# Optimization experiments

Measured on AMD Instinct MI355X. Metric: run time of the kernel, lower is better.

The kernel has to match this reference:

```python
import jax, jax.numpy as jnp
import numpy as np

N = 65536      # nodes (256x256 grid)
E = 1048576    # edges (avg degree 16)
T_IN = 10      # TIME_STEPS_IN
L = 64         # LATENT_DIMS
MID = 128      # LATENT_DIMS * MLP_RATIO
GD = 2         # grid dims


def _lin_init(key, fan_in, fan_out):
    kw, kb = jax.random.split(key)
    s = 1.0 / np.sqrt(fan_in)
    W = jax.random.uniform(kw, (fan_in, fan_out), jnp.float32, -s, s)
    b = jax.random.uniform(kb, (fan_out,), jnp.float32, -s, s)
    return W, b


def setup_inputs() -> dict:
    key = jax.random.key(0)
    ks = jax.random.split(key, 10)
    x = jax.random.normal(ks[0], (N, T_IN), jnp.float32)
    grid = jax.random.uniform(ks[1], (N, GD), jnp.float32)
    edge_index = jax.random.randint(ks[2], (2, E), 0, N, jnp.int64)
    W_proj1, b_proj1 = _lin_init(ks[3], T_IN + GD, MID)
    W_proj2, b_proj2 = _lin_init(ks[4], MID, L)
    Wk, bk = _lin_init(ks[5], 2 * L + 2 * GD + 1, L)   # K edge MLP (single linear)
    Ww, bw = _lin_init(ks[6], L, L)                     # W node MLP (single linear)
    W_dec1, b_dec1 = _lin_init(ks[7], L, MID)
    W_dec2, b_dec2 = _lin_init(ks[8], MID, 1)
    return {"x": x, "grid": grid, "edge_index": edge_index,
            "W_proj1": W_proj1, "b_proj1": b_proj1, "W_proj2": W_proj2, "b_proj2": b_proj2,
            "Wk": Wk, "bk": bk, "Ww": Ww, "bw": bw,
            "W_dec1": W_dec1, "b_dec1": b_dec1, "W_dec2": W_dec2, "b_dec2": b_dec2}


def _gelu(x):
    return jax.nn.gelu(x, approximate=False)  # torch F.gelu default = exact erf


def reference(x, grid, edge_index, W_proj1, b_proj1, W_proj2, b_proj2,
              Wk, bk, Ww, bw, W_dec1, b_dec1, W_dec2, b_dec2):
    # project: cat(x, grid) -> Linear -> GELU -> Linear
    h = jnp.concatenate([x, grid], axis=-1)               # [N, T_IN+2]
    h = _gelu(h @ W_proj1 + b_proj1) @ W_proj2 + b_proj2  # [N, L]

    # message passing block (PyG source_to_target: j = row 0, i = row 1)
    src = edge_index[0]
    dst = edge_index[1]
    x_j = h[src]                                          # [E, L]
    x_i = h[dst]                                          # [E, L]
    g_j = grid[src]                                       # [E, 2]
    g_i = grid[dst]                                       # [E, 2]
    dist = jnp.sqrt(jnp.sum(jnp.square(g_i - g_j), axis=-1, keepdims=True))  # [E, 1]
    ef = jnp.concatenate([dist, g_i, g_j, x_i, x_j], axis=-1)  # [E, 2L+5]
    msg = ef @ Wk + bk                                    # [E, L]
    aggr = jax.ops.segment_sum(msg, dst, num_segments=N)  # [N, L]
    h = _gelu(h @ Ww + bw + aggr)                         # update

    # decode: Linear -> GELU -> Linear
    out = _gelu(h @ W_dec1 + b_dec1) @ W_dec2 + b_dec2    # [N, 1]
    return out
```

## Files before the change

kernel.cpp:

```cpp
#include <hip/hip_runtime.h>
#include <hip/hip_fp16.h>

static __device__ __forceinline__ float gelu(float x) {
    return 0.5f * x * (1.0f + erff(x * 0.70710678118654752f));
}

#define CAPR 32

typedef _Float16 v8h __attribute__((ext_vector_type(8)));
typedef float    v4f __attribute__((ext_vector_type(4)));
typedef int      v4i __attribute__((ext_vector_type(4)));
union F8 { uint4 u; v8h v; _Float16 f[8]; };

static __device__ __forceinline__ void acc8(float* a, uint4 u) {
    float2 f0 = __half22float2(*(__half2*)&u.x);
    float2 f1 = __half22float2(*(__half2*)&u.y);
    float2 f2 = __half22float2(*(__half2*)&u.z);
    float2 f3 = __half22float2(*(__half2*)&u.w);
    a[0] += f0.x; a[1] += f0.y; a[2] += f1.x; a[3] += f1.y;
    a[4] += f2.x; a[5] += f2.y; a[6] += f3.x; a[7] += f3.y;
}

static __device__ __forceinline__ uint4 pack8(const float* v) {
    __half2 p0 = __floats2half2_rn(v[0], v[1]);
    __half2 p1 = __floats2half2_rn(v[2], v[3]);
    __half2 p2 = __floats2half2_rn(v[4], v[5]);
    __half2 p3 = __floats2half2_rn(v[6], v[7]);
    uint4 u;
    u.x = *(unsigned*)&p0; u.y = *(unsigned*)&p1;
    u.z = *(unsigned*)&p2; u.w = *(unsigned*)&p3;
    return u;
}

__global__ void __launch_bounds__(256, 4)
k_enc_scat(const float* __restrict__ x,
           const float* __restrict__ grid,
           const float* __restrict__ W1,
           const float* __restrict__ b1,
           const float* __restrict__ W2,
           const float* __restrict__ b2,
           const int* __restrict__ ei, int* __restrict__ cnt,
           unsigned short* __restrict__ ssrc,
           __half* __restrict__ h16, int N, int E, int scatB)
{
    __shared__ uint4 tabW2[1024];
    __shared__ __half wmids[4 * 16 * 136];
    int tid = threadIdx.x;

    if ((int)blockIdx.x < scatB) {
        int p = blockIdx.x & 7;
        int c = blockIdx.x >> 3;
        const v4i* s4 = (const v4i*)ei;
        const v4i* d4 = (const v4i*)(ei + E);
        int g4 = (E / (scatB >> 3)) >> 2;
        int base4 = c * g4;
        int shift = 31 - __clz(N >> 3);
#pragma unroll 8
        for (int g = 0; g < g4 / 256; g++) {
            int idx = base4 + g * 256 + tid;
            v4i d = __builtin_nontemporal_load(&d4[idx]);
            v4i s = __builtin_nontemporal_load(&s4[idx]);
            int q;
            if ((d[0] >> shift) == p) {
                q = atomicAdd(&cnt[(d[0] << 1) + 0], 1);
                if (q < CAPR) ssrc[((size_t)d[0] << 6) + q] = (unsigned short)s[0];
            }
            if ((d[1] >> shift) == p) {
                q = atomicAdd(&cnt[(d[1] << 1) + 1], 1);
                if (q < CAPR) ssrc[((size_t)d[1] << 6) + 32 + q] = (unsigned short)s[1];
            }
            if ((d[2] >> shift) == p) {
                q = atomicAdd(&cnt[(d[2] << 1) + 0], 1);
                if (q < CAPR) ssrc[((size_t)d[2] << 6) + q] = (unsigned short)s[2];
            }
            if ((d[3] >> shift) == p) {
                q = atomicAdd(&cnt[(d[3] << 1) + 1], 1);
                if (q < CAPR) ssrc[((size_t)d[3] << 6) + 32 + q] = (unsigned short)s[3];
            }
        }
        return;
    }

    int eb = blockIdx.x - scatB;
    int lane = tid & 63, wave = tid >> 6;
    int m = lane & 15, quad = lane >> 4;

    F8 w1f[8];
#pragma unroll
    for (int nt = 0; nt < 8; nt++) {
        int col = nt * 16 + m;
        int k0 = quad << 3;
#pragma unroll
        for (int j = 0; j < 8; j++)
            w1f[nt].f[j] = (k0 + j < 12) ? (_Float16)W1[(k0 + j) * 128 + col] : (_Float16)0.f;
    }

    for (int idx = tid; idx < 1024; idx += 256) {
        int l2 = idx & 63, nt = (idx >> 6) & 3, kc = idx >> 8;
        int col = nt * 16 + (l2 & 15);
        int k0 = kc * 32 + ((l2 >> 4) << 3);
        F8 f;
#pragma unroll
        for (int j = 0; j < 8; j++) f.f[j] = (_Float16)W2[(k0 + j) * 64 + col];
        tabW2[idx] = f.u;
    }
    __syncthreads();

    __half* wm = &wmids[wave * 16 * 136];

    for (int t = 0; t < 2; t++) {
        int tile = eb * 8 + wave * 2 + t;
        int base = tile * 16;
        int n = base + m;
        F8 a1;
#pragma unroll
        for (int j = 0; j < 8; j++) a1.f[j] = (_Float16)0.f;
        if (quad == 0) {
            float2 x0 = *(const float2*)&x[(size_t)n * 10 + 0];
            float2 x1 = *(const float2*)&x[(size_t)n * 10 + 2];
            float2 x2 = *(const float2*)&x[(size_t)n * 10 + 4];
            float2 x3 = *(const float2*)&x[(size_t)n * 10 + 6];
            a1.f[0] = (_Float16)x0.x; a1.f[1] = (_Float16)x0.y;
            a1.f[2] = (_Float16)x1.x; a1.f[3] = (_Float16)x1.y;
            a1.f[4] = (_Float16)x2.x; a1.f[5] = (_Float16)x2.y;
            a1.f[6] = (_Float16)x3.x; a1.f[7] = (_Float16)x3.y;
        } else if (quad == 1) {
            float2 x4 = *(const float2*)&x[(size_t)n * 10 + 8];
            float2 g  = *(const float2*)&grid[(size_t)n * 2];
            a1.f[0] = (_Float16)x4.x; a1.f[1] = (_Float16)x4.y;
            a1.f[2] = (_Float16)g.x;  a1.f[3] = (_Float16)g.y;
        }
#pragma unroll
        for (int nt = 0; nt < 8; nt++) {
            int col = nt * 16 + m;
            float b = b1[col];
            v4f acc = {b, b, b, b};
            acc = __builtin_amdgcn_mfma_f32_16x16x32_f16(a1.v, w1f[nt].v, acc, 0, 0, 0);
#pragma unroll
            for (int reg = 0; reg < 4; reg++)
                wm[(quad * 4 + reg) * 136 + col] = __float2half(gelu(acc[reg]));
        }
        __syncthreads();

        F8 a2[4];
#pragma unroll
        for (int kc = 0; kc < 4; kc++)
            a2[kc].u = *(const uint4*)&wm[m * 136 + kc * 32 + quad * 8];
#pragma unroll
        for (int nt = 0; nt < 4; nt++) {
            int col = nt * 16 + m;
            float b = b2[col];
            v4f acc = {b, b, b, b};
#pragma unroll
            for (int kc = 0; kc < 4; kc++) {
                F8 bf; bf.u = tabW2[kc * 256 + nt * 64 + lane];
                acc = __builtin_amdgcn_mfma_f32_16x16x32_f16(a2[kc].v, bf.v, acc, 0, 0, 0);
            }
#pragma unroll
            for (int reg = 0; reg < 4; reg++)
                h16[(size_t)(base + quad * 4 + reg) * 64 + col] = __float2half(acc[reg]);
        }
        __syncthreads();
    }
}

__global__ void __launch_bounds__(256, 1)
k_gupdec(const __half* __restrict__ h16,
         const unsigned short* __restrict__ ssrc,
         const int* __restrict__ cnt, const float* __restrict__ grid,
         const float* __restrict__ Wk, const float* __restrict__ bk,
         const float* __restrict__ Ww, const float* __restrict__ bw,
         const float* __restrict__ Wd1, const float* __restrict__ bd1,
         const float* __restrict__ Wd2, const float* __restrict__ bd2,
         float* __restrict__ out, int N)
{
    __shared__ uint4 tabW[512];
    __shared__ uint4 tabC[512];
    __shared__ uint4 tabD[512];
    __shared__ uint4 tabE[1024];
    __shared__ __half h2t[4 * 16 * 72];
    int tid = threadIdx.x;
    int lane = tid & 63, wave = tid >> 6;
    int m = lane & 15, quad = lane >> 4;

    for (int idx = tid; idx < 512; idx += 256) {
        int l2 = idx & 63, nt = (idx >> 6) & 3, kc = idx >> 8;
        int col = nt * 16 + (l2 & 15);
        int kr  = kc * 32 + ((l2 >> 4) << 3);
        F8 fw, fc, fd;
#pragma unroll
        for (int j = 0; j < 8; j++) {
            fw.f[j] = (_Float16)Ww[(kr + j) * 64 + col];
            fc.f[j] = (_Float16)Wk[(size_t)(5 + kr + j) * 64 + col];
            fd.f[j] = (_Float16)Wk[(size_t)(69 + kr + j) * 64 + col];
        }
        tabW[idx] = fw.u; tabC[idx] = fc.u; tabD[idx] = fd.u;
    }
    for (int idx = tid; idx < 1024; idx += 256) {
        int l2 = idx & 63, nt = (idx >> 6) & 7, kc = idx >> 9;
        int col = nt * 16 + (l2 & 15);
        int kr  = kc * 32 + ((l2 >> 4) << 3);
        F8 f;
#pragma unroll
        for (int j = 0; j < 8; j++) f.f[j] = (_Float16)Wd1[(kr + j) * 128 + col];
        tabE[idx] = f.u;
    }
    F8 vreg[4];
#pragma unroll
    for (int nt = 0; nt < 4; nt++) {
        int col = nt * 16 + m;
#pragma unroll
        for (int j = 0; j < 8; j++) vreg[nt].f[j] = (_Float16)0.f;
        if (quad == 0) {
            vreg[nt].f[0] = (_Float16)bw[col];
            vreg[nt].f[1] = (_Float16)bk[col];
            vreg[nt].f[2] = (_Float16)Wk[col];
            vreg[nt].f[3] = (_Float16)Wk[64 + col];
            vreg[nt].f[4] = (_Float16)Wk[128 + col];
            vreg[nt].f[5] = (_Float16)Wk[192 + col];
            vreg[nt].f[6] = (_Float16)Wk[256 + col];
        }
    }
    __syncthreads();

    const uint4* h8 = (const uint4*)h16;
    __half* wt = &h2t[wave * 16 * 72];
    float bd2v = bd2[0];

    int tile = blockIdx.x * 4 + wave;
    int base = tile * 16;
    int n = base + m;
    int2 cv = *(const int2*)&cnt[n << 1];
    float gix0 = grid[2 * n], giy0 = grid[2 * n + 1];

    float a0[8] = {0,0,0,0,0,0,0,0};
    float a1g[8] = {0,0,0,0,0,0,0,0};
    float sgx = 0.f, sgy = 0.f, sd = 0.f;
#pragma unroll
    for (int r = 0; r < 2; r++) {
        int dg = min((r == 0) ? cv.x : cv.y, CAPR);
        const unsigned short* sr = ssrc + ((size_t)n << 6) + (r << 5);
        for (int i = 0; i < dg; i += 4) {
            ushort4 sv = *(const ushort4*)&sr[i];
            int sx = sv.x, sy = sv.y, sz = sv.z, sw = sv.w;
            int rem = dg - i;
            if (rem < 4) {
                if (rem <= 1) sy = sx;
                if (rem <= 2) sz = sx;
                sw = (rem <= 3) ? sx : sw;
            }
            uint4 u;
            u = h8[(size_t)sx * 8 + quad];     acc8(a0, u);
            u = h8[(size_t)sx * 8 + 4 + quad]; acc8(a1g, u);
            if (rem > 1) {
                u = h8[(size_t)sy * 8 + quad];     acc8(a0, u);
                u = h8[(size_t)sy * 8 + 4 + quad]; acc8(a1g, u);
            }
            if (rem > 2) {
                u = h8[(size_t)sz * 8 + quad];     acc8(a0, u);
                u = h8[(size_t)sz * 8 + 4 + quad]; acc8(a1g, u);
            }
            if (rem > 3) {
                u = h8[(size_t)sw * 8 + quad];     acc8(a0, u);
                u = h8[(size_t)sw * 8 + 4 + quad]; acc8(a1g, u);
            }
            if (i + quad < dg) {
                int sj = (quad == 0) ? sx : (quad == 1) ? sy : (quad == 2) ? sz : sw;
                float2 g = *(const float2*)&grid[2 * sj];
                float dx = gix0 - g.x, dy = giy0 - g.y;
                sd += sqrtf(dx * dx + dy * dy);
                sgx += g.x; sgy += g.y;
            }
        }
    }
    sd  += __shfl_xor(sd, 16);  sd  += __shfl_xor(sd, 32);
    sgx += __shfl_xor(sgx, 16); sgx += __shfl_xor(sgx, 32);
    sgy += __shfl_xor(sgy, 16); sgy += __shfl_xor(sgy, 32);

    float deg = (float)(min(cv.x, CAPR) + min(cv.y, CAPR));
    float gix = gix0 * deg, giy = giy0 * deg;

    F8 ah0, ah1, as0, as1, ahd0, ahd1, au;
    ah0.u = h8[(size_t)n * 8 + quad];
    ah1.u = h8[(size_t)n * 8 + 4 + quad];
    as0.u = pack8(a0);
    as1.u = pack8(a1g);
    _Float16 dh = (_Float16)deg;
#pragma unroll
    for (int j = 0; j < 8; j++) { ahd0.f[j] = ah0.f[j] * dh; ahd1.f[j] = ah1.f[j] * dh; }
    float z = (quad == 0) ? 1.f : 0.f;
    au.f[0] = (_Float16)z;          au.f[1] = (_Float16)(deg * z);
    au.f[2] = (_Float16)(sd * z);   au.f[3] = (_Float16)(gix * z);
    au.f[4] = (_Float16)(giy * z);  au.f[5] = (_Float16)(sgx * z);
    au.f[6] = (_Float16)(sgy * z);  au.f[7] = (_Float16)0.f;

#pragma unroll
    for (int nt = 0; nt < 4; nt++) {
        F8 bw0, bw1, bc0, bc1, bd0, bd1f;
        bw0.u = tabW[nt * 64 + lane];       bw1.u = tabW[256 + nt * 64 + lane];
        bc0.u = tabC[nt * 64 + lane];       bc1.u = tabC[256 + nt * 64 + lane];
        bd0.u = tabD[nt * 64 + lane];       bd1f.u = tabD[256 + nt * 64 + lane];
        v4f acc = {0.f, 0.f, 0.f, 0.f};
        acc = __builtin_amdgcn_mfma_f32_16x16x32_f16(au.v,   vreg[nt].v, acc, 0, 0, 0);
        acc = __builtin_amdgcn_mfma_f32_16x16x32_f16(ah0.v,  bw0.v,  acc, 0, 0, 0);
        acc = __builtin_amdgcn_mfma_f32_16x16x32_f16(ah1.v,  bw1.v,  acc, 0, 0, 0);
        acc = __builtin_amdgcn_mfma_f32_16x16x32_f16(ahd0.v, bc0.v,  acc, 0, 0, 0);
        acc = __builtin_amdgcn_mfma_f32_16x16x32_f16(ahd1.v, bc1.v,  acc, 0, 0, 0);
        acc = __builtin_amdgcn_mfma_f32_16x16x32_f16(as0.v,  bd0.v,  acc, 0, 0, 0);
        acc = __builtin_amdgcn_mfma_f32_16x16x32_f16(as1.v,  bd1f.v, acc, 0, 0, 0);
#pragma unroll
        for (int reg = 0; reg < 4; reg++)
            wt[(quad * 4 + reg) * 72 + m + 16 * nt] = __float2half(gelu(acc[reg]));
    }
    __syncthreads();

    F8 dh0, dh1;
    dh0.u = *(const uint4*)&wt[m * 72 + quad * 8];
    dh1.u = *(const uint4*)&wt[m * 72 + 32 + quad * 8];
    float p[4] = {0.f, 0.f, 0.f, 0.f};
#pragma unroll
    for (int nt = 0; nt < 8; nt++) {
        int col = m + 16 * nt;
        float b = bd1[col];
        float w2 = Wd2[col];
        F8 b0, b1;
        b0.u = tabE[nt * 64 + lane];
        b1.u = tabE[512 + nt * 64 + lane];
        v4f acc = {b, b, b, b};
        acc = __builtin_amdgcn_mfma_f32_16x16x32_f16(dh0.v, b0.v, acc, 0, 0, 0);
        acc = __builtin_amdgcn_mfma_f32_16x16x32_f16(dh1.v, b1.v, acc, 0, 0, 0);
#pragma unroll
        for (int reg = 0; reg < 4; reg++) p[reg] += gelu(acc[reg]) * w2;
    }
#pragma unroll
    for (int reg = 0; reg < 4; reg++) {
        p[reg] += __shfl_xor(p[reg], 1);
        p[reg] += __shfl_xor(p[reg], 2);
        p[reg] += __shfl_xor(p[reg], 4);
        p[reg] += __shfl_xor(p[reg], 8);
    }
    if (m == 0) {
#pragma unroll
        for (int reg = 0; reg < 4; reg++)
            out[base + quad * 4 + reg] = p[reg] + bd2v;
    }
}

extern "C" void kernel_launch(void* const* d_in, const int* in_sizes, int n_in,
                              void* d_out, int out_size, void* d_ws, size_t ws_size,
                              hipStream_t stream)
{
    const float* x    = (const float*)d_in[0];
    const float* grid = (const float*)d_in[1];
    const int*   ei   = (const int*)d_in[2];
    const float* W1   = (const float*)d_in[3];
    const float* b1   = (const float*)d_in[4];
    const float* W2   = (const float*)d_in[5];
    const float* b2   = (const float*)d_in[6];
    const float* Wk   = (const float*)d_in[7];
    const float* bk   = (const float*)d_in[8];
    const float* Ww   = (const float*)d_in[9];
    const float* bw   = (const float*)d_in[10];
    const float* Wd1  = (const float*)d_in[11];
    const float* bd1  = (const float*)d_in[12];
    const float* Wd2  = (const float*)d_in[13];
    const float* bd2  = (const float*)d_in[14];
    float* out = (float*)d_out;

    int N = in_sizes[0] / 10;
    int E = in_sizes[2] / 2;

    char* ws = (char*)d_ws;
    size_t o_h16  = 0;
    size_t o_cnt  = o_h16 + (size_t)N * 64 * 2;
    size_t o_ssrc = o_cnt + (size_t)N * 2 * 4;

    __half* h16 = (__half*)(ws + o_h16);
    int*    cnt = (int*)  (ws + o_cnt);
    unsigned short* ssrc = (unsigned short*)(ws + o_ssrc);

    hipMemsetAsync(cnt, 0, (size_t)N * 2 * 4, stream);

    int scatB = E / (256 * 4);
    int encB  = (N / 16) / 8;
    k_enc_scat<<<dim3(scatB + encB), dim3(256), 0, stream>>>(x, grid, W1, b1, W2, b2,
                                                             ei, cnt, ssrc, h16, N, E, scatB);
    int tiles = N / 16;
    k_gupdec<<<dim3(tiles / 4), dim3(256), 0, stream>>>(h16, ssrc, cnt, grid,
                                                        Wk, bk, Ww, bw,
                                                        Wd1, bd1, Wd2, bd2, out, N);
}
```

Measured before the change: 224.8 us.

## Precompute fp16 MFMA weight tables once in global memory for update kernel

Adds an extra block to the encoder/scatter kernel that converts Ww, Wk, Wd1 and the bias/geometry vector into fp16 MFMA fragment tables in workspace memory. The update/decode kernel now reads these fragments straight from global memory (L2-resident) rather than rebuilding them in LDS in every block with strided fp32 loads and a barrier. The update kernel also drops its LDS tables and raises its launch bounds to four blocks per CU to improve occupancy. The trade-off is repeated global/L2 fragment loads inside the MFMA loops in place of LDS reads, plus possible register pressure from the tighter launch bound.

Result: faster. 201.0 us (median of 2 runs) (-10.6%).

```diff
diff --git a/kernel.cpp b/kernel.cpp
--- a/kernel.cpp
+++ b/kernel.cpp
@@ -41,7 +41,11 @@
            const float* __restrict__ b2,
            const int* __restrict__ ei, int* __restrict__ cnt,
            unsigned short* __restrict__ ssrc,
-           __half* __restrict__ h16, int N, int E, int scatB)
+           __half* __restrict__ h16,
+           const float* __restrict__ Wk, const float* __restrict__ bk,
+           const float* __restrict__ Ww, const float* __restrict__ bw,
+           const float* __restrict__ Wd1, uint4* __restrict__ gtab,
+           int N, int E, int scatB, int encB)
 {
     __shared__ uint4 tabW2[1024];
     __shared__ __half wmids[4 * 16 * 136];
@@ -81,6 +85,54 @@
         return;
     }
 
+    if ((int)blockIdx.x == scatB + encB) {
+        uint4* gW = gtab;
+        uint4* gC = gtab + 512;
+        uint4* gD = gtab + 1024;
+        uint4* gE = gtab + 1536;
+        uint4* gV = gtab + 2560;
+        for (int idx = tid; idx < 512; idx += 256) {
+            int l2 = idx & 63, nt = (idx >> 6) & 3, kc = idx >> 8;
+            int col = nt * 16 + (l2 & 15);
+            int kr  = kc * 32 + ((l2 >> 4) << 3);
+            F8 fw, fc, fd;
+#pragma unroll
+            for (int j = 0; j < 8; j++) {
+                fw.f[j] = (_Float16)Ww[(kr + j) * 64 + col];
+                fc.f[j] = (_Float16)Wk[(size_t)(5 + kr + j) * 64 + col];
+                fd.f[j] = (_Float16)Wk[(size_t)(69 + kr + j) * 64 + col];
+            }
+            gW[idx] = fw.u; gC[idx] = fc.u; gD[idx] = fd.u;
+        }
+        for (int idx = tid; idx < 1024; idx += 256) {
+            int l2 = idx & 63, nt = (idx >> 6) & 7, kc = idx >> 9;
+            int col = nt * 16 + (l2 & 15);
+            int kr  = kc * 32 + ((l2 >> 4) << 3);
+            F8 f;
+#pragma unroll
+            for (int j = 0; j < 8; j++) f.f[j] = (_Float16)Wd1[(kr + j) * 128 + col];
+            gE[idx] = f.u;
+        }
+        {
+            int l2 = tid & 63, nt = tid >> 6;
+            int col = nt * 16 + (l2 & 15);
+            F8 fv;
+#pragma unroll
+            for (int j = 0; j < 8; j++) fv.f[j] = (_Float16)0.f;
+            if ((l2 >> 4) == 0) {
+                fv.f[0] = (_Float16)bw[col];
+                fv.f[1] = (_Float16)bk[col];
+                fv.f[2] = (_Float16)Wk[col];
+                fv.f[3] = (_Float16)Wk[64 + col];
+                fv.f[4] = (_Float16)Wk[128 + col];
+                fv.f[5] = (_Float16)Wk[192 + col];
+                fv.f[6] = (_Float16)Wk[256 + col];
+            }
+            gV[tid] = fv.u;
+        }
+        return;
+    }
+
     int eb = blockIdx.x - scatB;
     int lane = tid & 63, wave = tid >> 6;
     int m = lane & 15, quad = lane >> 4;
@@ -164,64 +216,25 @@
     }
 }
 
-__global__ void __launch_bounds__(256, 1)
+__global__ void __launch_bounds__(256, 4)
 k_gupdec(const __half* __restrict__ h16,
          const unsigned short* __restrict__ ssrc,
          const int* __restrict__ cnt, const float* __restrict__ grid,
-         const float* __restrict__ Wk, const float* __restrict__ bk,
-         const float* __restrict__ Ww, const float* __restrict__ bw,
-         const float* __restrict__ Wd1, const float* __restrict__ bd1,
-         const float* __restrict__ Wd2, const float* __restrict__ bd2,
+         const uint4* __restrict__ gtab,
+         const float* __restrict__ bd1, const float* __restrict__ Wd2,
+         const float* __restrict__ bd2,
          float* __restrict__ out, int N)
 {
-    __shared__ uint4 tabW[512];
-    __shared__ uint4 tabC[512];
-    __shared__ uint4 tabD[512];
-    __shared__ uint4 tabE[1024];
     __shared__ __half h2t[4 * 16 * 72];
     int tid = threadIdx.x;
     int lane = tid & 63, wave = tid >> 6;
     int m = lane & 15, quad = lane >> 4;
 
-    for (int idx = tid; idx < 512; idx += 256) {
-        int l2 = idx & 63, nt = (idx >> 6) & 3, kc = idx >> 8;
-        int col = nt * 16 + (l2 & 15);
-        int kr  = kc * 32 + ((l2 >> 4) << 3);
-        F8 fw, fc, fd;
-#pragma unroll
-        for (int j = 0; j < 8; j++) {
-            fw.f[j] = (_Float16)Ww[(kr + j) * 64 + col];
-            fc.f[j] = (_Float16)Wk[(size_t)(5 + kr + j) * 64 + col];
-            fd.f[j] = (_Float16)Wk[(size_t)(69 + kr + j) * 64 + col];
-        }
-        tabW[idx] = fw.u; tabC[idx] = fc.u; tabD[idx] = fd.u;
-    }
-    for (int idx = tid; idx < 1024; idx += 256) {
-        int l2 = idx & 63, nt = (idx >> 6) & 7, kc = idx >> 9;
-        int col = nt * 16 + (l2 & 15);
-        int kr  = kc * 32 + ((l2 >> 4) << 3);
-        F8 f;
-#pragma unroll
-        for (int j = 0; j < 8; j++) f.f[j] = (_Float16)Wd1[(kr + j) * 128 + col];
-        tabE[idx] = f.u;
-    }
-    F8 vreg[4];
-#pragma unroll
-    for (int nt = 0; nt < 4; nt++) {
-        int col = nt * 16 + m;
-#pragma unroll
-        for (int j = 0; j < 8; j++) vreg[nt].f[j] = (_Float16)0.f;
-        if (quad == 0) {
-            vreg[nt].f[0] = (_Float16)bw[col];
-            vreg[nt].f[1] = (_Float16)bk[col];
-            vreg[nt].f[2] = (_Float16)Wk[col];
-            vreg[nt].f[3] = (_Float16)Wk[64 + col];
-            vreg[nt].f[4] = (_Float16)Wk[128 + col];
-            vreg[nt].f[5] = (_Float16)Wk[192 + col];
-            vreg[nt].f[6] = (_Float16)Wk[256 + col];
-        }
-    }
-    __syncthreads();
+    const uint4* gW = gtab;
+    const uint4* gC = gtab + 512;
+    const uint4* gD = gtab + 1024;
+    const uint4* gE = gtab + 1536;
+    const uint4* gV = gtab + 2560;
 
     const uint4* h8 = (const uint4*)h16;
     __half* wt = &h2t[wave * 16 * 72];
@@ -296,12 +309,13 @@
 
 #pragma unroll
     for (int nt = 0; nt < 4; nt++) {
-        F8 bw0, bw1, bc0, bc1, bd0, bd1f;
-        bw0.u = tabW[nt * 64 + lane];       bw1.u = tabW[256 + nt * 64 + lane];
-        bc0.u = tabC[nt * 64 + lane];       bc1.u = tabC[256 + nt * 64 + lane];
-        bd0.u = tabD[nt * 64 + lane];       bd1f.u = tabD[256 + nt * 64 + lane];
+        F8 bv, bw0, bw1, bc0, bc1, bd0, bd1f;
+        bv.u  = gV[nt * 64 + lane];
+        bw0.u = gW[nt * 64 + lane];       bw1.u = gW[256 + nt * 64 + lane];
+        bc0.u = gC[nt * 64 + lane];       bc1.u = gC[256 + nt * 64 + lane];
+        bd0.u = gD[nt * 64 + lane];       bd1f.u = gD[256 + nt * 64 + lane];
         v4f acc = {0.f, 0.f, 0.f, 0.f};
-        acc = __builtin_amdgcn_mfma_f32_16x16x32_f16(au.v,   vreg[nt].v, acc, 0, 0, 0);
+        acc = __builtin_amdgcn_mfma_f32_16x16x32_f16(au.v,   bv.v,   acc, 0, 0, 0);
         acc = __builtin_amdgcn_mfma_f32_16x16x32_f16(ah0.v,  bw0.v,  acc, 0, 0, 0);
         acc = __builtin_amdgcn_mfma_f32_16x16x32_f16(ah1.v,  bw1.v,  acc, 0, 0, 0);
         acc = __builtin_amdgcn_mfma_f32_16x16x32_f16(ahd0.v, bc0.v,  acc, 0, 0, 0);
@@ -324,8 +338,8 @@
         float b = bd1[col];
         float w2 = Wd2[col];
         F8 b0, b1;
-        b0.u = tabE[nt * 64 + lane];
-        b1.u = tabE[512 + nt * 64 + lane];
+        b0.u = gE[nt * 64 + lane];
+        b1.u = gE[512 + nt * 64 + lane];
         v4f acc = {b, b, b, b};
         acc = __builtin_amdgcn_mfma_f32_16x16x32_f16(dh0.v, b0.v, acc, 0, 0, 0);
         acc = __builtin_amdgcn_mfma_f32_16x16x32_f16(dh1.v, b1.v, acc, 0, 0, 0);
@@ -374,19 +388,22 @@
     size_t o_h16  = 0;
     size_t o_cnt  = o_h16 + (size_t)N * 64 * 2;
     size_t o_ssrc = o_cnt + (size_t)N * 2 * 4;
+    size_t o_tab  = o_ssrc + (size_t)N * 64 * 2;
 
     __half* h16 = (__half*)(ws + o_h16);
     int*    cnt = (int*)  (ws + o_cnt);
     unsigned short* ssrc = (unsigned short*)(ws + o_ssrc);
+    uint4*  gtab = (uint4*)(ws + o_tab);
 
     hipMemsetAsync(cnt, 0, (size_t)N * 2 * 4, stream);
 
     int scatB = E / (256 * 4);
     int encB  = (N / 16) / 8;
-    k_enc_scat<<<dim3(scatB + encB), dim3(256), 0, stream>>>(x, grid, W1, b1, W2, b2,
-                                                             ei, cnt, ssrc, h16, N, E, scatB);
+    k_enc_scat<<<dim3(scatB + encB + 1), dim3(256), 0, stream>>>(x, grid, W1, b1, W2, b2,
+                                                                 ei, cnt, ssrc, h16,
+                                                                 Wk, bk, Ww, bw, Wd1, gtab,
+                                                                 N, E, scatB, encB);
     int tiles = N / 16;
-    k_gupdec<<<dim3(tiles / 4), dim3(256), 0, stream>>>(h16, ssrc, cnt, grid,
-                                                        Wk, bk, Ww, bw,
-                                                        Wd1, bd1, Wd2, bd2, out, N);
-}
+    k_gupdec<<<dim3(tiles / 4), dim3(256), 0, stream>>>(h16, ssrc, cnt, grid, gtab,
+                                                        bd1, Wd2, bd2, out, N);
+}
```
